# Kernel tuning notes

Measured on AMD Instinct MI355X. Metric: run time of the kernel, lower is better.

Reference implementation:

```python
import jax, jax.numpy as jnp
import numpy as np

N_NODES = 100000
N_EDGES = 1600000
N_GRAPHS = 64
EMB_DIM = 64
DIMS = [6, 16, 32, 64, EMB_DIM]


def setup_inputs() -> dict:
    key = jax.random.key(0)
    ks = jax.random.split(key, 16)
    feat = jax.random.normal(ks[0], (N_NODES, DIMS[0]), dtype=jnp.float32)
    src = jax.random.randint(ks[1], (N_EDGES,), 0, N_NODES)
    dst = jax.random.randint(ks[2], (N_EDGES,), 0, N_NODES)
    graph_ids = jnp.sort(jax.random.randint(ks[3], (N_NODES,), 0, N_GRAPHS))
    inp = {"feat": feat, "src": src, "dst": dst, "graph_ids": graph_ids}
    # fc_neigh weights for each SAGEConv (gcn aggregator has no fc_self), Xavier-ish init
    for i in range(4):
        din, dout = DIMS[i], DIMS[i + 1]
        scale = 1.0 / np.sqrt(din)
        inp[f"W{i+1}"] = jax.random.uniform(ks[4 + 2 * i], (din, dout), jnp.float32, -scale, scale)
        inp[f"b{i+1}"] = jnp.zeros((dout,), jnp.float32)
    return inp


def _sage_gcn(feat, src, dst, deg, W, b):
    # DGL SAGEConv aggregator_type='gcn':
    # h_neigh = (sum_{u in N(v)} h_u + h_v) / (in_deg(v) + 1); out = h_neigh @ W + b
    neigh = jax.ops.segment_sum(feat[src], dst, num_segments=N_NODES)  # [N, din]
    h = (neigh + feat) / (deg[:, None] + 1.0)
    return h @ W + b


def reference(feat, src, dst, graph_ids, W1, b1, W2, b2, W3, b3, W4, b4):
    deg = jax.ops.segment_sum(jnp.ones((N_EDGES,), feat.dtype), dst, num_segments=N_NODES)
    h = feat
    for W, b in ((W1, b1), (W2, b2), (W3, b3), (W4, b4)):
        h = jax.nn.relu(_sage_gcn(h, src, dst, deg, W, b))
    # dgl.mean_nodes: per-graph mean over nodes
    sums = jax.ops.segment_sum(h, graph_ids, num_segments=N_GRAPHS)          # [G, emb]
    cnts = jax.ops.segment_sum(jnp.ones((N_NODES,), h.dtype), graph_ids, num_segments=N_GRAPHS)
    return sums / jnp.maximum(cnts, 1.0)[:, None]
```

## Files before the change

### kernel.cpp

```cpp
#include <hip/hip_runtime.h>
#include <hip/hip_bf16.h>
#include <hip/hip_fp16.h>

#define N_NODES 100000
#define N_EDGES 1600000
#define N_GRAPHS 64

#define NB_BKT 256
#define NPBKT 391
#define EPB 4096
#define NBLK_FEAT ((N_NODES + 255) / 256)
#define NBLK_BIN ((N_EDGES + EPB - 1) / EPB)
#define BKT_CAP 7168


__device__ __forceinline__ __half2 u2h(unsigned int u) {
    return __builtin_bit_cast(__half2, u);
}
__device__ __forceinline__ float2 u2f2(unsigned int u) {
    return __half22float2(u2h(u));
}
__device__ __forceinline__ unsigned int packh2(float a, float b) {
    return __builtin_bit_cast(unsigned int, __float22half2_rn(make_float2(a, b)));
}


__global__ __launch_bounds__(256) void prep(const float* __restrict__ feat,
                                            const int* __restrict__ dst,
                                            const int* __restrict__ src,
                                            uint4* __restrict__ feat16,
                                            int* __restrict__ gcur,
                                            uint2* __restrict__ rec, int n, int E) {
    __shared__ int cnt[NB_BKT];
    __shared__ int lbase[NB_BKT];
    __shared__ int gofs[NB_BKT];
    __shared__ uint2 stage[EPB];
    int t = threadIdx.x;

    if ((int)blockIdx.x < NBLK_FEAT) {
        __shared__ float sf[256 * 6];
        int b0 = blockIdx.x * 256;
        int c = min(256, n - b0) * 6;
        for (int i = t; i < c; i += 256) sf[i] = feat[(size_t)b0 * 6 + i];
        __syncthreads();
        int v = b0 + t;
        if (v < n) {
            const float* f = sf + t * 6;
            uint4 r;
            r.x = packh2(f[0], f[1]);
            r.y = packh2(f[2], f[3]);
            r.z = packh2(f[4], f[5]);
            r.w = 0u;
            feat16[v] = r;
        }
        return;
    }

    int e0 = (blockIdx.x - NBLK_FEAT) * EPB;
    cnt[t] = 0;
    __syncthreads();
    int myb[16], mypos[16];
    unsigned myd[16], mys[16];
#pragma unroll
    for (int k = 0; k < 16; ++k) {
        int e = e0 + k * 256 + t;
        if (e < E) {
            unsigned d = (unsigned)dst[e];
            int b = (int)(d / (unsigned)NPBKT);
            myd[k] = d;
            mys[k] = (unsigned)src[e];
            myb[k] = b;
            mypos[k] = atomicAdd(&cnt[b], 1);
        } else {
            myb[k] = -1;
        }
    }
    __syncthreads();
    int c = cnt[t];
    int res = (c > 0) ? atomicAdd(&gcur[t], c) : 0;
    lbase[t] = c;
    __syncthreads();
    for (int o = 1; o < 256; o <<= 1) {
        int a = (t >= o) ? lbase[t - o] : 0;
        __syncthreads();
        lbase[t] += a;
        __syncthreads();
    }
    lbase[t] -= c;
    gofs[t] = res;
    __syncthreads();
#pragma unroll
    for (int k = 0; k < 16; ++k)
        if (myb[k] >= 0) stage[lbase[myb[k]] + mypos[k]] = make_uint2(myd[k], mys[k]);
    __syncthreads();
    int total = min(EPB, E - e0);
    for (int i = t; i < total; i += 256) {
        int lo = 0, hi = NB_BKT - 1;
        while (lo < hi) {
            int m = (lo + hi + 1) >> 1;
            if (lbase[m] <= i) lo = m; else hi = m - 1;
        }
        rec[(size_t)lo * BKT_CAP + gofs[lo] + (i - lbase[lo])] = stage[i];
    }
}


__global__ __launch_bounds__(256) void fill_bucket(const uint2* __restrict__ rec,
                                                   const int* __restrict__ gcur,
                                                   int* __restrict__ rp,
                                                   int* __restrict__ col, int n) {
    __shared__ int sdeg[512];
    __shared__ int lcur[512];
    __shared__ int sg[256];
    __shared__ int lcol[8192];
    int p = blockIdx.x, t = threadIdx.x;
    int nbase = p * NPBKT;
    int nn = min(NPBKT, n - nbase);
    int g = gcur[t];
    sg[t] = g;
    __syncthreads();
    for (int o = 1; o < 256; o <<= 1) {
        int a = (t >= o) ? sg[t - o] : 0;
        __syncthreads();
        sg[t] += a;
        __syncthreads();
    }
    int ex = sg[t] - g;
    __syncthreads();
    sg[t] = ex;
    __syncthreads();
    int cbase = sg[p];
    int cnt = gcur[p];
    sdeg[t] = 0;
    sdeg[t + 256] = 0;
    __syncthreads();
    const uint2* r = rec + (size_t)p * BKT_CAP;
    for (int i = t; i < cnt; i += 256) atomicAdd(&sdeg[r[i].x - (unsigned)nbase], 1);
    __syncthreads();
    int c0 = sdeg[t], c1 = sdeg[t + 256];
    for (int o = 1; o < 512; o <<= 1) {
        int a = (t >= o) ? sdeg[t - o] : 0;
        int b = (t + 256 >= o) ? sdeg[t + 256 - o] : 0;
        __syncthreads();
        sdeg[t] += a;
        sdeg[t + 256] += b;
        __syncthreads();
    }
    int ex0 = sdeg[t] - c0, ex1 = sdeg[t + 256] - c1;
    lcur[t] = ex0;
    lcur[t + 256] = ex1;
    if (t < nn) rp[nbase + t] = cbase + ex0;
    if (t + 256 < nn) rp[nbase + t + 256] = cbase + ex1;
    if (p == NB_BKT - 1 && t == 0) rp[n] = cbase + cnt;
    __syncthreads();
    for (int i = t; i < cnt; i += 256) {
        uint2 e = r[i];
        int slot = atomicAdd(&lcur[e.x - (unsigned)nbase], 1);
        lcol[slot] = (int)e.y;
    }
    __syncthreads();
    for (int i = t; i < cnt; i += 256) col[cbase + i] = lcol[i];
}


template <int DIN, int DOUT>
__global__ __launch_bounds__(256) void sage_f16(const uint4* __restrict__ hin,
                                                const int* __restrict__ rp,
                                                const int* __restrict__ col,
                                                const float* __restrict__ W,
                                                const float* __restrict__ bias,
                                                unsigned int* __restrict__ hout,
                                                int real_din, int n) {
    constexpr int WPN = DIN / 8;
    constexpr int NPB = 256 / WPN;
    constexpr int OPT = DOUT / WPN;
    __shared__ float sW[DIN * DOUT];
    __shared__ float sB[DOUT];
    __shared__ float sH[NPB][DIN + 1];

    int tid = threadIdx.x;
    for (int i = tid; i < DIN * DOUT; i += 256) sW[i] = (i < real_din * DOUT) ? W[i] : 0.f;
    if (tid < DOUT) sB[tid] = bias[tid];

    int sub = tid / WPN;
    int t = tid % WPN;
    int v = blockIdx.x * NPB + sub;

    if (v < n) {
        int r0 = rp[v], r1 = rp[v + 1];
        const __half2 z = __float2half2_rn(0.f);
        __half2 acc[4][4];
#pragma unroll
        for (int s = 0; s < 4; ++s)
#pragma unroll
            for (int q = 0; q < 4; ++q) acc[s][q] = z;
        int j = r0;
        for (; j + 8 <= r1; j += 8) {
            uint4 w[8];
#pragma unroll
            for (int k = 0; k < 8; ++k) w[k] = hin[col[j + k] * WPN + t];
#pragma unroll
            for (int k = 0; k < 8; ++k) {
                __half2* a = acc[k & 3];
                a[0] = __hadd2(a[0], u2h(w[k].x));
                a[1] = __hadd2(a[1], u2h(w[k].y));
                a[2] = __hadd2(a[2], u2h(w[k].z));
                a[3] = __hadd2(a[3], u2h(w[k].w));
            }
        }
        for (; j + 4 <= r1; j += 4) {
            uint4 w[4];
#pragma unroll
            for (int k = 0; k < 4; ++k) w[k] = hin[col[j + k] * WPN + t];
#pragma unroll
            for (int k = 0; k < 4; ++k) {
                __half2* a = acc[k];
                a[0] = __hadd2(a[0], u2h(w[k].x));
                a[1] = __hadd2(a[1], u2h(w[k].y));
                a[2] = __hadd2(a[2], u2h(w[k].z));
                a[3] = __hadd2(a[3], u2h(w[k].w));
            }
        }
        for (; j < r1; ++j) {
            uint4 w = hin[col[j] * WPN + t];
            acc[0][0] = __hadd2(acc[0][0], u2h(w.x));
            acc[0][1] = __hadd2(acc[0][1], u2h(w.y));
            acc[0][2] = __hadd2(acc[0][2], u2h(w.z));
            acc[0][3] = __hadd2(acc[0][3], u2h(w.w));
        }
#pragma unroll
        for (int q = 0; q < 4; ++q)
            acc[0][q] = __hadd2(__hadd2(acc[0][q], acc[1][q]),
                                __hadd2(acc[2][q], acc[3][q]));
        uint4 ws = hin[v * WPN + t];
        unsigned swd[4] = {ws.x, ws.y, ws.z, ws.w};
        float inv = 1.0f / (float)(r1 - r0 + 1);
#pragma unroll
        for (int q = 0; q < 4; ++q) {
            float2 f = __half22float2(acc[0][q]);
            float2 s = u2f2(swd[q]);
            sH[sub][t * 8 + 2 * q + 0] = (f.x + s.x) * inv;
            sH[sub][t * 8 + 2 * q + 1] = (f.y + s.y) * inv;
        }
    }
    __syncthreads();
    if (v < n) {
        int o0 = t * OPT;
        float accO[OPT];
#pragma unroll
        for (int i = 0; i < OPT; ++i) accO[i] = sB[o0 + i];
#pragma unroll 4
        for (int k = 0; k < DIN; ++k) {
            float hk = sH[sub][k];
#pragma unroll
            for (int i = 0; i < OPT; ++i) accO[i] += hk * sW[k * DOUT + o0 + i];
        }
        unsigned wds[OPT / 2];
#pragma unroll
        for (int i = 0; i < OPT; i += 2)
            wds[i / 2] = packh2(fmaxf(accO[i], 0.f), fmaxf(accO[i + 1], 0.f));
        unsigned* op = hout + v * (DOUT / 2) + o0 / 2;
        if constexpr (OPT / 2 == 4) {
            *reinterpret_cast<uint4*>(op) = make_uint4(wds[0], wds[1], wds[2], wds[3]);
        } else if constexpr (OPT / 2 == 8) {
            reinterpret_cast<uint4*>(op)[0] = make_uint4(wds[0], wds[1], wds[2], wds[3]);
            reinterpret_cast<uint4*>(op)[1] = make_uint4(wds[4], wds[5], wds[6], wds[7]);
        } else {
            *reinterpret_cast<uint2*>(op) = make_uint2(wds[0], wds[1]);
        }
    }
}


__device__ __forceinline__ int lower_bound_i(const int* __restrict__ a, int n, int key) {
    int lo = 0, hi = n;
    while (lo < hi) {
        int m = (lo + hi) >> 1;
        if (a[m] < key) lo = m + 1; else hi = m;
    }
    return lo;
}

__global__ __launch_bounds__(256) void pool_f16(const unsigned int* __restrict__ h32,
                                                const int* __restrict__ gids,
                                                float* __restrict__ out, int n) {
    int bx = blockIdx.x;
    int g = bx >> 3, s = bx & 7;
    int start = lower_bound_i(gids, n, g);
    int end = lower_bound_i(gids, n, g + 1);
    int len = end - start;
    float inv = 1.0f / (float)(len > 0 ? len : 1);
    int chunk = (len + 7) / 8;
    int s0 = start + s * chunk;
    int s1 = min(s0 + chunk, end);
    int t = threadIdx.x;
    int d = t & 31, j = t >> 5;
    float a0 = 0.f, a1 = 0.f;
    for (int i = s0 + j; i < s1; i += 8) {
        float2 f = u2f2(h32[(size_t)i * 32 + d]);
        a0 += f.x;
        a1 += f.y;
    }
    __shared__ float red[8][32][2];
    red[j][d][0] = a0;
    red[j][d][1] = a1;
    __syncthreads();
    if (t < 64) {
        int dd = t & 31, e = t >> 5;
        float tot = 0.f;
#pragma unroll
        for (int k = 0; k < 8; ++k) tot += red[k][dd][e];
        atomicAdd(&out[g * 64 + 2 * dd + e], tot * inv);
    }
}


extern "C" void kernel_launch(void* const* d_in, const int* in_sizes, int n_in,
                              void* d_out, int out_size, void* d_ws, size_t ws_size,
                              hipStream_t stream) {
    const int N = N_NODES, E = N_EDGES;
    const float* feat = (const float*)d_in[0];
    const int* src = (const int*)d_in[1];
    const int* dst = (const int*)d_in[2];
    const int* gids = (const int*)d_in[3];
    const float* W1 = (const float*)d_in[4];
    const float* b1 = (const float*)d_in[5];
    const float* W2 = (const float*)d_in[6];
    const float* b2 = (const float*)d_in[7];
    const float* W3 = (const float*)d_in[8];
    const float* b3 = (const float*)d_in[9];
    const float* W4 = (const float*)d_in[10];
    const float* b4 = (const float*)d_in[11];
    float* out = (float*)d_out;

    int* rp = (int*)d_ws;
    int* gcur = rp + (N + 1);
    int* col = gcur + 256;
    size_t off = (size_t)((char*)(col + E) - (char*)d_ws);
    off = (off + 255) & ~(size_t)255;
    unsigned int* h1 = (unsigned int*)((char*)d_ws + off);
    unsigned int* h2 = h1 + (size_t)N * 8;
    unsigned int* h3 = h2 + (size_t)N * 16;
    unsigned int* h4 = h3 + (size_t)N * 32;
    uint4* feat16 = (uint4*)(h4 + (size_t)N * 32);
    uint2* rec = (uint2*)h3;

    hipMemsetAsync(out, 0, (size_t)N_GRAPHS * 64 * sizeof(float), stream);
    hipMemsetAsync(gcur, 0, 256 * sizeof(int), stream);

    prep<<<NBLK_FEAT + NBLK_BIN, 256, 0, stream>>>(feat, dst, src, feat16, gcur, rec, N, E);
    fill_bucket<<<NB_BKT, 256, 0, stream>>>(rec, gcur, rp, col, N);

    sage_f16<8, 16><<<(N + 255) / 256, 256, 0, stream>>>(
        feat16, rp, col, W1, b1, h1, 6, N);
    sage_f16<16, 32><<<(N + 127) / 128, 256, 0, stream>>>(
        (const uint4*)h1, rp, col, W2, b2, h2, 16, N);
    sage_f16<32, 64><<<(N + 63) / 64, 256, 0, stream>>>(
        (const uint4*)h2, rp, col, W3, b3, h3, 32, N);
    sage_f16<64, 64><<<(N + 31) / 32, 256, 0, stream>>>(
        (const uint4*)h3, rp, col, W4, b4, h4, 64, N);

    pool_f16<<<N_GRAPHS * 8, 256, 0, stream>>>(h4, gids, out, N);
}
```

Before: 186.8 us.

## Split each node's neighbor gather across two thread halves with 512-thread blocks

Each SAGE layer kernel now uses 512-thread blocks where two halves of the block gather alternating 8-edge chunks of the same node's neighbor list. The halves write half-precision partial sums to shared memory, and then all 512 threads share the dense matmul, with the degree normalization applied there. This doubles memory-level parallelism per node in the latency-bound gather and halves per-thread matmul outputs. The costs are larger blocks, a tighter launch bound that may cap registers, and a less efficient tail loop.

```diff
diff --git a/kernel.cpp b/kernel.cpp
--- a/kernel.cpp
+++ b/kernel.cpp
@@ -16,6 +16,9 @@
 
 __device__ __forceinline__ __half2 u2h(unsigned int u) {
     return __builtin_bit_cast(__half2, u);
+}
+__device__ __forceinline__ unsigned int h2u(__half2 h) {
+    return __builtin_bit_cast(unsigned int, h);
 }
 __device__ __forceinline__ float2 u2f2(unsigned int u) {
     return __half22float2(u2h(u));
@@ -164,109 +167,114 @@
 
 
 template <int DIN, int DOUT>
-__global__ __launch_bounds__(256) void sage_f16(const uint4* __restrict__ hin,
-                                                const int* __restrict__ rp,
-                                                const int* __restrict__ col,
-                                                const float* __restrict__ W,
-                                                const float* __restrict__ bias,
-                                                unsigned int* __restrict__ hout,
-                                                int real_din, int n) {
+__global__ __launch_bounds__(512, 8) void sage_split(const uint4* __restrict__ hin,
+                                                     const int* __restrict__ rp,
+                                                     const int* __restrict__ col,
+                                                     const float* __restrict__ W,
+                                                     const float* __restrict__ bias,
+                                                     unsigned int* __restrict__ hout,
+                                                     int real_din, int n) {
     constexpr int WPN = DIN / 8;
-    constexpr int NPB = 256 / WPN;
-    constexpr int OPT = DOUT / WPN;
+    constexpr int NPB = 512 / (2 * WPN);
+    constexpr int TPN2 = 2 * WPN;
+    constexpr int OPT = DOUT / TPN2;
     __shared__ float sW[DIN * DOUT];
     __shared__ float sB[DOUT];
-    __shared__ float sH[NPB][DIN + 1];
+    __shared__ unsigned sH[2][NPB][DIN / 2];
+    __shared__ float sInv[NPB];
 
     int tid = threadIdx.x;
-    for (int i = tid; i < DIN * DOUT; i += 256) sW[i] = (i < real_din * DOUT) ? W[i] : 0.f;
+    for (int i = tid; i < DIN * DOUT; i += 512) sW[i] = (i < real_din * DOUT) ? W[i] : 0.f;
     if (tid < DOUT) sB[tid] = bias[tid];
 
-    int sub = tid / WPN;
-    int t = tid % WPN;
+    int half = tid >> 8;
+    int t256 = tid & 255;
+    int sub = t256 / WPN;
+    int t = t256 % WPN;
     int v = blockIdx.x * NPB + sub;
 
     if (v < n) {
         int r0 = rp[v], r1 = rp[v + 1];
+        uint4 ws = make_uint4(0u, 0u, 0u, 0u);
+        if (half == 0) ws = hin[v * WPN + t];
         const __half2 z = __float2half2_rn(0.f);
         __half2 acc[4][4];
 #pragma unroll
         for (int s = 0; s < 4; ++s)
 #pragma unroll
             for (int q = 0; q < 4; ++q) acc[s][q] = z;
-        int j = r0;
-        for (; j + 8 <= r1; j += 8) {
-            uint4 w[8];
-#pragma unroll
-            for (int k = 0; k < 8; ++k) w[k] = hin[col[j + k] * WPN + t];
-#pragma unroll
-            for (int k = 0; k < 8; ++k) {
-                __half2* a = acc[k & 3];
-                a[0] = __hadd2(a[0], u2h(w[k].x));
-                a[1] = __hadd2(a[1], u2h(w[k].y));
-                a[2] = __hadd2(a[2], u2h(w[k].z));
-                a[3] = __hadd2(a[3], u2h(w[k].w));
+
+        for (int j = r0 + 8 * half; j < r1; j += 16) {
+            int m = r1 - j;
+            if (m >= 8) {
+                uint4 w[8];
+#pragma unroll
+                for (int k = 0; k < 8; ++k) w[k] = hin[col[j + k] * WPN + t];
+#pragma unroll
+                for (int k = 0; k < 8; ++k) {
+                    __half2* a = acc[k & 3];
+                    a[0] = __hadd2(a[0], u2h(w[k].x));
+                    a[1] = __hadd2(a[1], u2h(w[k].y));
+                    a[2] = __hadd2(a[2], u2h(w[k].z));
+                    a[3] = __hadd2(a[3], u2h(w[k].w));
+                }
+            } else {
+                for (int k = 0; k < m; ++k) {
+                    uint4 w = hin[col[j + k] * WPN + t];
+                    __half2* a = acc[k & 3];
+                    a[0] = __hadd2(a[0], u2h(w.x));
+                    a[1] = __hadd2(a[1], u2h(w.y));
+                    a[2] = __hadd2(a[2], u2h(w.z));
+                    a[3] = __hadd2(a[3], u2h(w.w));
+                }
             }
         }
-        for (; j + 4 <= r1; j += 4) {
-            uint4 w[4];
-#pragma unroll
-            for (int k = 0; k < 4; ++k) w[k] = hin[col[j + k] * WPN + t];
-#pragma unroll
-            for (int k = 0; k < 4; ++k) {
-                __half2* a = acc[k];
-                a[0] = __hadd2(a[0], u2h(w[k].x));
-                a[1] = __hadd2(a[1], u2h(w[k].y));
-                a[2] = __hadd2(a[2], u2h(w[k].z));
-                a[3] = __hadd2(a[3], u2h(w[k].w));
-            }
-        }
-        for (; j < r1; ++j) {
-            uint4 w = hin[col[j] * WPN + t];
-            acc[0][0] = __hadd2(acc[0][0], u2h(w.x));
-            acc[0][1] = __hadd2(acc[0][1], u2h(w.y));
-            acc[0][2] = __hadd2(acc[0][2], u2h(w.z));
-            acc[0][3] = __hadd2(acc[0][3], u2h(w.w));
-        }
+        __half2 a0[4];
 #pragma unroll
         for (int q = 0; q < 4; ++q)
-            acc[0][q] = __hadd2(__hadd2(acc[0][q], acc[1][q]),
-                                __hadd2(acc[2][q], acc[3][q]));
-        uint4 ws = hin[v * WPN + t];
-        unsigned swd[4] = {ws.x, ws.y, ws.z, ws.w};
-        float inv = 1.0f / (float)(r1 - r0 + 1);
-#pragma unroll
-        for (int q = 0; q < 4; ++q) {
-            float2 f = __half22float2(acc[0][q]);
-            float2 s = u2f2(swd[q]);
-            sH[sub][t * 8 + 2 * q + 0] = (f.x + s.x) * inv;
-            sH[sub][t * 8 + 2 * q + 1] = (f.y + s.y) * inv;
-        }
-    }
-    __syncthreads();
-    if (v < n) {
-        int o0 = t * OPT;
+            a0[q] = __hadd2(__hadd2(acc[0][q], acc[1][q]), __hadd2(acc[2][q], acc[3][q]));
+        if (half == 0) {
+            unsigned swd[4] = {ws.x, ws.y, ws.z, ws.w};
+#pragma unroll
+            for (int q = 0; q < 4; ++q) a0[q] = __hadd2(a0[q], u2h(swd[q]));
+            if (t == 0) sInv[sub] = 1.0f / (float)(r1 - r0 + 1);
+        }
+#pragma unroll
+        for (int q = 0; q < 4; ++q) sH[half][sub][t * 4 + q] = h2u(a0[q]);
+    }
+    __syncthreads();
+
+    int g_sub = tid / TPN2;
+    int g_t = tid % TPN2;
+    int gv = blockIdx.x * NPB + g_sub;
+    if (gv < n) {
+        float inv = sInv[g_sub];
+        int o0 = g_t * OPT;
         float accO[OPT];
 #pragma unroll
         for (int i = 0; i < OPT; ++i) accO[i] = sB[o0 + i];
 #pragma unroll 4
-        for (int k = 0; k < DIN; ++k) {
-            float hk = sH[sub][k];
-#pragma unroll
-            for (int i = 0; i < OPT; ++i) accO[i] += hk * sW[k * DOUT + o0 + i];
+        for (int kp = 0; kp < DIN / 2; ++kp) {
+            float2 f0 = u2f2(sH[0][g_sub][kp]);
+            float2 f1 = u2f2(sH[1][g_sub][kp]);
+            float hx = (f0.x + f1.x) * inv;
+            float hy = (f0.y + f1.y) * inv;
+            const float* w0 = sW + (2 * kp) * DOUT + o0;
+            const float* w1 = sW + (2 * kp + 1) * DOUT + o0;
+#pragma unroll
+            for (int i = 0; i < OPT; ++i) accO[i] += hx * w0[i] + hy * w1[i];
         }
         unsigned wds[OPT / 2];
 #pragma unroll
         for (int i = 0; i < OPT; i += 2)
             wds[i / 2] = packh2(fmaxf(accO[i], 0.f), fmaxf(accO[i + 1], 0.f));
-        unsigned* op = hout + v * (DOUT / 2) + o0 / 2;
+        unsigned* op = hout + gv * (DOUT / 2) + o0 / 2;
         if constexpr (OPT / 2 == 4) {
             *reinterpret_cast<uint4*>(op) = make_uint4(wds[0], wds[1], wds[2], wds[3]);
-        } else if constexpr (OPT / 2 == 8) {
-            reinterpret_cast<uint4*>(op)[0] = make_uint4(wds[0], wds[1], wds[2], wds[3]);
-            reinterpret_cast<uint4*>(op)[1] = make_uint4(wds[4], wds[5], wds[6], wds[7]);
+        } else if constexpr (OPT / 2 == 2) {
+            *reinterpret_cast<uint2*>(op) = make_uint2(wds[0], wds[1]);
         } else {
-            *reinterpret_cast<uint2*>(op) = make_uint2(wds[0], wds[1]);
+            *op = wds[0];
         }
     }
 }
@@ -351,13 +359,13 @@
     prep<<<NBLK_FEAT + NBLK_BIN, 256, 0, stream>>>(feat, dst, src, feat16, gcur, rec, N, E);
     fill_bucket<<<NB_BKT, 256, 0, stream>>>(rec, gcur, rp, col, N);
 
-    sage_f16<8, 16><<<(N + 255) / 256, 256, 0, stream>>>(
+    sage_split<8, 16><<<(N + 255) / 256, 512, 0, stream>>>(
         feat16, rp, col, W1, b1, h1, 6, N);
-    sage_f16<16, 32><<<(N + 127) / 128, 256, 0, stream>>>(
+    sage_split<16, 32><<<(N + 127) / 128, 512, 0, stream>>>(
         (const uint4*)h1, rp, col, W2, b2, h2, 16, N);
-    sage_f16<32, 64><<<(N + 63) / 64, 256, 0, stream>>>(
+    sage_split<32, 64><<<(N + 63) / 64, 512, 0, stream>>>(
         (const uint4*)h2, rp, col, W3, b3, h3, 32, N);
-    sage_f16<64, 64><<<(N + 31) / 32, 256, 0, stream>>>(
+    sage_split<64, 64><<<(N + 31) / 32, 512, 0, stream>>>(
         (const uint4*)h3, rp, col, W4, b4, h4, 64, N);
 
     pool_f16<<<N_GRAPHS * 8, 256, 0, stream>>>(h4, gids, out, N);
```

After: 327.4 us. 1.75x slower.
